# Performance work log

Measured on AMD Instinct MI355X. Metric: run time of the kernel, lower is better.

Reference implementation:

```python
import jax, jax.numpy as jnp
import numpy as np

# ---- static config (mirrors torch __init__ kwargs) ----
DIM, DEPTH, HEADS, DHEAD, MLP = 1024, 5, 8, 128, 2048
INNER = HEADS * DHEAD
RADIUS, K, SS, TKS, TS = 0.7, 16, 8, 3, 2
B, T, N = 2, 8, 2048
M = N // SS
JN = 17
EPS = 1e-5


def _ln(x, s, b):
    m = x.mean(-1, keepdims=True)
    v = ((x - m) ** 2).mean(-1, keepdims=True)
    return (x - m) * jax.lax.rsqrt(v + EPS) * s + b


def _fps(xyz, m):
    # farthest point sampling, pointnet2 semantics (first pick = index 0)
    # xyz: [BF, n, 3] -> [BF, m] int32
    BF, n, _ = xyz.shape
    d0 = jnp.full((BF, n), 1e10, xyz.dtype)
    i0 = jnp.zeros((BF,), jnp.int32)

    def body(carry, _):
        dist, last = carry
        p = jnp.take_along_axis(xyz, jnp.broadcast_to(last[:, None, None], (BF, 1, 3)), 1)
        dist = jnp.minimum(dist, jnp.sum((xyz - p) ** 2, -1))
        nxt = jnp.argmax(dist, -1).astype(jnp.int32)
        return (dist, nxt), nxt

    _, rest = jax.lax.scan(body, (d0, i0), None, length=m - 1)
    return jnp.concatenate([i0[None], rest], 0).T  # [BF, m]


def _forward(radar, conv_d_w, conv_f_w, pos_w, pos_b, joint_template, joint_pos,
             ln1_s, ln1_b, qkv_w, out_w, out_b, ln2_s, ln2_b,
             ff_w1, ff_b1, ff_w2, ff_b2,
             red_ln_s, red_ln_b, red_w1, red_b1, red_w2, red_b2,
             head_ln_s, head_ln_b, head_w1, head_b1, head_w2, head_b2):
    Bv = radar.shape[0]
    xyz, fea = radar[..., :3], radar[..., 3:]
    # ---- P4DConv tube embedding ----
    # temporal replicate padding [1, 0]
    xyz_p = jnp.concatenate([xyz[:, :1], xyz], 1)   # [B,T+1,N,3]
    fea_p = jnp.concatenate([fea[:, :1], fea], 1)
    centers = np.arange(1, (T + 1) - 1, TS)          # anchor frame indices (static)
    Tq = len(centers)
    offs = np.array([-1, 0, 1])                      # temporal kernel offsets (tks=3)
    cxyz = xyz_p[:, centers].reshape(Bv * Tq, N, 3)
    aidx = _fps(cxyz, M)                             # [B*Tq, M]
    anchors = jnp.take_along_axis(
        cxyz, jnp.broadcast_to(aidx[..., None], (Bv * Tq, M, 3)), 1
    ).reshape(Bv, Tq, M, 3)
    nx = jnp.stack([xyz_p[:, centers + o] for o in offs], 2)  # [B,Tq,3,N,3]
    nf = jnp.stack([fea_p[:, centers + o] for o in offs], 2)  # [B,Tq,3,N,3]
    # ball query: first-K indices with d2 < r^2 (in point order), padded with the
    # first hit; 0 if no hit -- matches pointnet2 CUDA semantics
    sg = jax.lax.stop_gradient
    d2 = jnp.sum((sg(anchors)[:, :, None, :, None, :] - sg(nx)[:, :, :, None, :, :]) ** 2, -1)
    cand = jnp.where(d2 < RADIUS ** 2, jnp.arange(N, dtype=jnp.int32), N)
    cand = jnp.sort(cand, -1)[..., :K]               # [B,Tq,3,M,K]
    first = cand[..., :1]
    idx = jnp.where(cand < N, cand, first)
    idx = jnp.where(first < N, idx, 0)
    BF = Bv * Tq * 3
    idxf = jnp.broadcast_to(idx.reshape(BF, M * K, 1), (BF, M * K, 3))
    gx = jnp.take_along_axis(nx.reshape(BF, N, 3), idxf, 1).reshape(Bv, Tq, 3, M, K, 3)
    gf = jnp.take_along_axis(nf.reshape(BF, N, 3), idxf, 1).reshape(Bv, Tq, 3, M, K, 3)
    disp = gx - anchors[:, :, None, :, None, :]
    tdisp = jnp.broadcast_to(
        jnp.asarray(offs, jnp.float32)[None, None, :, None, None, None],
        disp.shape[:-1] + (1,))
    # conv_d(displacement) + conv_f(features): fused single 1x1 conv (no bias)
    w = jnp.concatenate([conv_d_w, conv_f_w], 1)     # [DIM, 7]
    feat = jnp.einsum('btomkc,dc->btomkd', jnp.concatenate([disp, tdisp, gf], -1), w)
    feat = feat.max(4).max(2)                        # spatial max, temporal max -> [B,Tq,M,DIM]
    # ---- P4Transformer forward ----
    tt = jnp.broadcast_to(jnp.arange(1, Tq + 1, dtype=jnp.float32)[None, :, None, None],
                          (Bv, Tq, M, 1))
    xyzts = jnp.concatenate([anchors, tt], -1).reshape(Bv, Tq * M, 4)
    features = feat.reshape(Bv, Tq * M, DIM)
    emb = xyzts @ pos_w.T + pos_b + features         # pos_embedding is a 1x1 Conv1d
    joints = jnp.broadcast_to(joint_template[None] + joint_pos, (Bv, JN, DIM))
    x = jnp.concatenate([joints, emb], 1)            # [B, 17 + Tq*M, DIM]
    S = x.shape[1]
    scale = DHEAD ** -0.5
    for l in range(DEPTH):
        h = _ln(x, ln1_s[l], ln1_b[l])
        q, k, v = jnp.split(h @ qkv_w[l], 3, -1)
        q = q.reshape(Bv, S, HEADS, DHEAD).transpose(0, 2, 1, 3)
        k = k.reshape(Bv, S, HEADS, DHEAD).transpose(0, 2, 1, 3)
        v = v.reshape(Bv, S, HEADS, DHEAD).transpose(0, 2, 1, 3)
        att = jax.nn.softmax(jnp.einsum('bhid,bhjd->bhij', q, k) * scale, -1)
        o = jnp.einsum('bhij,bhjd->bhid', att, v).transpose(0, 2, 1, 3).reshape(Bv, S, INNER)
        x = x + o @ out_w[l] + out_b[l]
        h = _ln(x, ln2_s[l], ln2_b[l])
        x = x + jax.nn.gelu(h @ ff_w1[l] + ff_b1[l], approximate=False) @ ff_w2[l] + ff_b2[l]
    j = x[:, :JN]
    j64 = jax.nn.relu(_ln(j, red_ln_s, red_ln_b) @ red_w1 + red_b1) @ red_w2 + red_b2
    out = jax.nn.relu(_ln(j64, head_ln_s, head_ln_b) @ head_w1 + head_b1) @ head_w2 + head_b2
    # torch returns (output, None, joint_embed_out, radar_feature, radar_position);
    # None is dropped here
    return out, j64, features, xyzts


def setup_inputs():
    key = jax.random.key(0)
    ks = iter(jax.random.split(key, 40))

    def nrm(shape, fan_in):
        return jax.random.normal(next(ks), shape, jnp.float32) / float(np.sqrt(fan_in))

    inp = {}
    inp['radar'] = jax.random.normal(next(ks), (B, T, N, 6), jnp.float32)
    inp['conv_d_w'] = nrm((DIM, 4), 4)
    inp['conv_f_w'] = nrm((DIM, 3), 3)
    inp['pos_w'] = nrm((DIM, 4), 4)
    inp['pos_b'] = jnp.zeros((DIM,), jnp.float32)
    inp['joint_template'] = jax.random.uniform(next(ks), (JN, DIM), jnp.float32)
    i = np.arange(JN)[:, None]
    j = np.arange(DIM)[None, :]
    ang = i / 10000.0 ** ((j - (j % 2)) / DIM)
    inp['joint_pos'] = jnp.asarray(np.where(j % 2 == 0, np.sin(ang), np.cos(ang))[None],
                                   jnp.float32)
    inp['ln1_s'] = jnp.ones((DEPTH, DIM), jnp.float32)
    inp['ln1_b'] = jnp.zeros((DEPTH, DIM), jnp.float32)
    inp['qkv_w'] = nrm((DEPTH, DIM, 3 * INNER), DIM)
    inp['out_w'] = nrm((DEPTH, INNER, DIM), INNER)
    inp['out_b'] = jnp.zeros((DEPTH, DIM), jnp.float32)
    inp['ln2_s'] = jnp.ones((DEPTH, DIM), jnp.float32)
    inp['ln2_b'] = jnp.zeros((DEPTH, DIM), jnp.float32)
    inp['ff_w1'] = nrm((DEPTH, DIM, MLP), DIM)
    inp['ff_b1'] = jnp.zeros((DEPTH, MLP), jnp.float32)
    inp['ff_w2'] = nrm((DEPTH, MLP, DIM), MLP)
    inp['ff_b2'] = jnp.zeros((DEPTH, DIM), jnp.float32)
    inp['red_ln_s'] = jnp.ones((DIM,), jnp.float32)
    inp['red_ln_b'] = jnp.zeros((DIM,), jnp.float32)
    inp['red_w1'] = nrm((DIM, 512), DIM)
    inp['red_b1'] = jnp.zeros((512,), jnp.float32)
    inp['red_w2'] = nrm((512, 64), 512)
    inp['red_b2'] = jnp.zeros((64,), jnp.float32)
    inp['head_ln_s'] = jnp.ones((64,), jnp.float32)
    inp['head_ln_b'] = jnp.zeros((64,), jnp.float32)
    inp['head_w1'] = nrm((64, 32), 64)
    inp['head_b1'] = jnp.zeros((32,), jnp.float32)
    inp['head_w2'] = nrm((32, 3), 32)
    inp['head_b2'] = jnp.zeros((3,), jnp.float32)
    return inp


def reference(radar, conv_d_w, conv_f_w, pos_w, pos_b, joint_template, joint_pos,
              ln1_s, ln1_b, qkv_w, out_w, out_b, ln2_s, ln2_b,
              ff_w1, ff_b1, ff_w2, ff_b2,
              red_ln_s, red_ln_b, red_w1, red_b1, red_w2, red_b2,
              head_ln_s, head_ln_b, head_w1, head_b1, head_w2, head_b2):
    return _forward(radar, conv_d_w, conv_f_w, pos_w, pos_b, joint_template, joint_pos,
                    ln1_s, ln1_b, qkv_w, out_w, out_b, ln2_s, ln2_b,
                    ff_w1, ff_b1, ff_w2, ff_b2,
                    red_ln_s, red_ln_b, red_w1, red_b1, red_w2, red_b2,
                    head_ln_s, head_ln_b, head_w1, head_b1, head_w2, head_b2)
```

## Files before the change

kernel.cpp:

```cpp
#include <hip/hip_runtime.h>
#include <hip/hip_bf16.h>

#define S_LEN 1041
#define ROWS  2082

__device__ __forceinline__ float d2chain(float dx, float dy, float dz) {
  float t = dx * dx;
  t = fmaf(dy, dy, t);
  t = fmaf(dz, dz, t);
  return t;
}

__device__ __forceinline__ float gelu_exact(float v) {
  return 0.5f * v * (1.0f + erff(v * 0.70710678118654752f));
}

__global__ __launch_bounds__(256) void fps_kernel(const float* __restrict__ radar,
                                                  float* __restrict__ anchors,
                                                  float* __restrict__ xyzts) {
  __shared__ float xs[2048], ys[2048], zs[2048];
  __shared__ int warr[256];
  __shared__ float rv[4];
  __shared__ int ri[4];
  int bf = blockIdx.x;
  int b = bf >> 2, tq = bf & 3;
  int f = 2 * tq;
  const float* base = radar + (size_t)(b * 8 + f) * 2048 * 6;
  int tid = threadIdx.x;
#pragma unroll
  for (int r = 0; r < 8; ++r) {
    int n = tid + r * 256;
    const float* p = base + (size_t)n * 6;
    xs[n] = p[0]; ys[n] = p[1]; zs[n] = p[2];
  }
  float dist[8];
#pragma unroll
  for (int r = 0; r < 8; ++r) dist[r] = 1e10f;
  if (tid == 0) warr[0] = 0;
  __syncthreads();
  int last = 0;
  for (int it = 1; it < 256; ++it) {
    float px = xs[last], py = ys[last], pz = zs[last];
    float bv = -1.0f; int bi = 0x7fffffff;
#pragma unroll
    for (int r = 0; r < 8; ++r) {
      int n = tid + r * 256;
      float d = fminf(dist[r], d2chain(xs[n] - px, ys[n] - py, zs[n] - pz));
      dist[r] = d;
      if (d > bv || (d == bv && n < bi)) { bv = d; bi = n; }
    }
#pragma unroll
    for (int o = 1; o < 64; o <<= 1) {
      float ov = __shfl_xor(bv, o);
      int   oi = __shfl_xor(bi, o);
      if (ov > bv || (ov == bv && oi < bi)) { bv = ov; bi = oi; }
    }
    if ((tid & 63) == 0) { rv[tid >> 6] = bv; ri[tid >> 6] = bi; }
    __syncthreads();
    if (tid == 0) {
      float fv = rv[0]; int fi = ri[0];
      for (int w = 1; w < 4; ++w)
        if (rv[w] > fv || (rv[w] == fv && ri[w] < fi)) { fv = rv[w]; fi = ri[w]; }
      warr[it] = fi;
    }
    __syncthreads();
    last = warr[it];
  }
  int m = tid;
  int a = warr[m];
  float ax = xs[a], ay = ys[a], az = zs[a];
  float* ap = anchors + (size_t)(bf * 256 + m) * 3;
  ap[0] = ax; ap[1] = ay; ap[2] = az;
  float* xp = xyzts + (size_t)(b * 1024 + tq * 256 + m) * 4;
  xp[0] = ax; xp[1] = ay; xp[2] = az; xp[3] = (float)(tq + 1);
}

__global__ __launch_bounds__(256) void radius_kernel(const float* __restrict__ radar,
                                                     const float* __restrict__ anchors,
                                                     int* __restrict__ nidx) {
  int r = blockIdx.x * 256 + threadIdx.x;
  int m = r & 255;
  int g = r >> 8;
  int o = g % 3;
  int bt = g / 3;
  int tq = bt & 3, b = bt >> 2;
  const float* ap = anchors + (size_t)(bt * 256 + m) * 3;
  float ax = ap[0], ay = ap[1], az = ap[2];
  int u = 2 * tq + o;
  int f = (u == 0) ? 0 : (u - 1);
  const float* base = radar + (size_t)(b * 8 + f) * 2048 * 6;
  size_t ob = (size_t)r * 16;
  int cnt = 0, first = 0;
  for (int n = 0; n < 2048; ++n) {
    const float* p = base + (size_t)n * 6;
    float t = d2chain(ax - p[0], ay - p[1], az - p[2]);
    if (t < 0.49f) {
      if (cnt == 0) first = n;
      nidx[ob + cnt] = n;
      if (++cnt == 16) break;
    }
  }
  for (int k = cnt; k < 16; ++k) nidx[ob + k] = first;
}

__global__ __launch_bounds__(256) void group_kernel(const float* __restrict__ radar,
                                                    const float* __restrict__ anchors,
                                                    const int* __restrict__ nidx,
                                                    const float* __restrict__ cdw,
                                                    const float* __restrict__ cfw,
                                                    const float* __restrict__ posw,
                                                    const float* __restrict__ posb,
                                                    float* __restrict__ feat,
                                                    float* __restrict__ x) {
  __shared__ float in7[48][8];
  int blk = blockIdx.x;
  int m = blk & 255, bt = blk >> 8;
  int tq = bt & 3, b = bt >> 2;
  int tid = threadIdx.x;
  float a0 = anchors[(size_t)blk * 3 + 0];
  float a1 = anchors[(size_t)blk * 3 + 1];
  float a2 = anchors[(size_t)blk * 3 + 2];
  if (tid < 48) {
    int o = tid >> 4;
    int k = tid & 15;
    int gi = nidx[((size_t)(bt * 3 + o) * 256 + m) * 16 + k];
    int u = 2 * tq + o;
    int f = (u == 0) ? 0 : (u - 1);
    const float* p = radar + ((size_t)(b * 8 + f) * 2048 + gi) * 6;
    in7[tid][0] = p[0] - a0;
    in7[tid][1] = p[1] - a1;
    in7[tid][2] = p[2] - a2;
    in7[tid][3] = (float)(o - 1);
    in7[tid][4] = p[3];
    in7[tid][5] = p[4];
    in7[tid][6] = p[5];
  }
  __syncthreads();
  float tt = (float)(tq + 1);
#pragma unroll
  for (int j = 0; j < 4; ++j) {
    int d = j * 256 + tid;
    float4 wd = *(const float4*)(cdw + (size_t)d * 4);
    float w4 = cfw[(size_t)d * 3 + 0];
    float w5 = cfw[(size_t)d * 3 + 1];
    float w6 = cfw[(size_t)d * 3 + 2];
    float best = -INFINITY;
    for (int c = 0; c < 48; ++c) {
      const float* e = in7[c];
      float t = e[0] * wd.x;
      t = fmaf(e[1], wd.y, t);
      t = fmaf(e[2], wd.z, t);
      t = fmaf(e[3], wd.w, t);
      t = fmaf(e[4], w4, t);
      t = fmaf(e[5], w5, t);
      t = fmaf(e[6], w6, t);
      best = fmaxf(best, t);
    }
    feat[(size_t)blk * 1024 + d] = best;
    float4 pw = *(const float4*)(posw + (size_t)d * 4);
    float e = fmaf(a0, pw.x, fmaf(a1, pw.y, fmaf(a2, pw.z, fmaf(tt, pw.w, posb[d]))));
    x[((size_t)(b * 1041 + 17) + tq * 256 + m) * 1024 + d] = e + best;
  }
}

__global__ __launch_bounds__(256) void joints_kernel(const float* __restrict__ jt,
                                                     const float* __restrict__ jp,
                                                     float* __restrict__ x) {
  int blk = blockIdx.x;
  int b = blk / 17, jj = blk % 17;
  int d = threadIdx.x * 4;
  float4 t = *(const float4*)(jt + (size_t)jj * 1024 + d);
  float4 p = *(const float4*)(jp + (size_t)jj * 1024 + d);
  float4 r;
  r.x = t.x + p.x; r.y = t.y + p.y; r.z = t.z + p.z; r.w = t.w + p.w;
  *(float4*)(x + ((size_t)(b * 1041 + jj)) * 1024 + d) = r;
}

__global__ __launch_bounds__(256) void ln_kernel(const float* __restrict__ x,
                                                 const float* __restrict__ s,
                                                 const float* __restrict__ b,
                                                 float* __restrict__ h) {
  __shared__ float red[8];
  int row = blockIdx.x;
  int tid = threadIdx.x;
  float4 v = *(const float4*)(x + (size_t)row * 1024 + tid * 4);
  float sum = (v.x + v.y) + (v.z + v.w);
#pragma unroll
  for (int o = 32; o > 0; o >>= 1) sum += __shfl_xor(sum, o);
  if ((tid & 63) == 0) red[tid >> 6] = sum;
  __syncthreads();
  float mean = (red[0] + red[1] + red[2] + red[3]) * (1.0f / 1024.0f);
  float dx = v.x - mean, dy = v.y - mean, dz = v.z - mean, dw = v.w - mean;
  float sq = (dx * dx + dy * dy) + (dz * dz + dw * dw);
#pragma unroll
  for (int o = 32; o > 0; o >>= 1) sq += __shfl_xor(sq, o);
  if ((tid & 63) == 0) red[4 + (tid >> 6)] = sq;
  __syncthreads();
  float var = (red[4] + red[5] + red[6] + red[7]) * (1.0f / 1024.0f);
  float rs = rsqrtf(var + 1e-5f);
  float4 sv = *(const float4*)(s + tid * 4);
  float4 bv = *(const float4*)(b + tid * 4);
  float4 out;
  out.x = dx * rs * sv.x + bv.x;
  out.y = dy * rs * sv.y + bv.y;
  out.z = dz * rs * sv.z + bv.z;
  out.w = dw * rs * sv.w + bv.w;
  *(float4*)(h + (size_t)row * 1024 + tid * 4) = out;
}

template <bool BIAS, bool RES, bool GACT>
__global__ __launch_bounds__(256) void gemm64(const float* __restrict__ A,
                                              const float* __restrict__ Bw,
                                              const float* __restrict__ bias,
                                              float* __restrict__ C,
                                              int M, int N, int K) {
  __shared__ float As[16][68];
  __shared__ float Bs[16][132];
  int tid = threadIdx.x;
  int tx = tid & 15, ty = tid >> 4;
  int m0 = blockIdx.y * 64, n0 = blockIdx.x * 128;
  float acc[4][8] = {};
  int arow = tid >> 2, ak = (tid & 3) * 4;
  int brow = tid >> 4, bcol = (tid & 15) * 8;
  bool aok = (m0 + arow) < M;
  const float* aptr = A + (size_t)(m0 + arow) * K + ak;
  const float* bptr = Bw + (size_t)brow * N + n0 + bcol;
  for (int k0 = 0; k0 < K; k0 += 16) {
    float4 av = aok ? *(const float4*)(aptr + k0) : make_float4(0.f, 0.f, 0.f, 0.f);
    float4 b0 = *(const float4*)(bptr + (size_t)k0 * N);
    float4 b1 = *(const float4*)(bptr + (size_t)k0 * N + 4);
    __syncthreads();
    As[ak + 0][arow] = av.x;
    As[ak + 1][arow] = av.y;
    As[ak + 2][arow] = av.z;
    As[ak + 3][arow] = av.w;
    *(float4*)&Bs[brow][bcol] = b0;
    *(float4*)&Bs[brow][bcol + 4] = b1;
    __syncthreads();
#pragma unroll
    for (int kk = 0; kk < 16; ++kk) {
      float4 a4 = *(const float4*)&As[kk][ty * 4];
      float4 x0 = *(const float4*)&Bs[kk][tx * 8];
      float4 x1 = *(const float4*)&Bs[kk][tx * 8 + 4];
      float am[4] = {a4.x, a4.y, a4.z, a4.w};
      float bn[8] = {x0.x, x0.y, x0.z, x0.w, x1.x, x1.y, x1.z, x1.w};
#pragma unroll
      for (int i = 0; i < 4; ++i)
#pragma unroll
        for (int j = 0; j < 8; ++j) acc[i][j] = fmaf(am[i], bn[j], acc[i][j]);
    }
  }
#pragma unroll
  for (int i = 0; i < 4; ++i) {
    int row = m0 + ty * 4 + i;
    if (row < M) {
      float* cp = C + (size_t)row * N + n0 + tx * 8;
#pragma unroll
      for (int j = 0; j < 8; ++j) {
        float v = acc[i][j];
        if (BIAS) v += bias[n0 + tx * 8 + j];
        if (GACT) v = gelu_exact(v);
        if (RES) v += cp[j];
        cp[j] = v;
      }
    }
  }
}

__global__ __launch_bounds__(256) void attn_kernel(const float* __restrict__ qkv,
                                                   float* __restrict__ o) {
  __shared__ float Ks[32][128];
  __shared__ float Vs[32][128];
  __shared__ float Sl[32][33];
  int bh = blockIdx.y;
  int b = bh >> 3, hh = bh & 7;
  int tid = threadIdx.x;
  int g = tid >> 3, l8 = tid & 7;
  int qi = blockIdx.x * 32 + g;
  bool qok = qi < S_LEN;
  const float* base = qkv + (size_t)b * S_LEN * 3072;
  float qv[16];
  if (qok) {
    const float4* qp = (const float4*)(base + (size_t)qi * 3072 + hh * 128 + l8 * 16);
    float4 q0 = qp[0], q1 = qp[1], q2 = qp[2], q3 = qp[3];
    qv[0] = q0.x; qv[1] = q0.y; qv[2] = q0.z; qv[3] = q0.w;
    qv[4] = q1.x; qv[5] = q1.y; qv[6] = q1.z; qv[7] = q1.w;
    qv[8] = q2.x; qv[9] = q2.y; qv[10] = q2.z; qv[11] = q2.w;
    qv[12] = q3.x; qv[13] = q3.y; qv[14] = q3.z; qv[15] = q3.w;
  } else {
#pragma unroll
    for (int j = 0; j < 16; ++j) qv[j] = 0.f;
  }
  float ov[16];
#pragma unroll
  for (int j = 0; j < 16; ++j) ov[j] = 0.f;
  float mrun = -INFINITY, lrun = 0.f;
  const float scale = 0.08838834764831845f;
  for (int j0 = 0; j0 < S_LEN; j0 += 32) {
    __syncthreads();
#pragma unroll
    for (int r = 0; r < 4; ++r) {
      int f4 = r * 256 + tid;
      int key = f4 >> 5;
      int c4 = (f4 & 31) * 4;
      int jj = j0 + key;
      float4 kv, vv;
      if (jj < S_LEN) {
        kv = *(const float4*)(base + (size_t)jj * 3072 + 1024 + hh * 128 + c4);
        vv = *(const float4*)(base + (size_t)jj * 3072 + 2048 + hh * 128 + c4);
      } else {
        kv = make_float4(0.f, 0.f, 0.f, 0.f);
        vv = make_float4(0.f, 0.f, 0.f, 0.f);
      }
      *(float4*)&Ks[key][c4] = kv;
      *(float4*)&Vs[key][c4] = vv;
    }
    __syncthreads();
    float tmax = -INFINITY;
    for (int jj = 0; jj < 32; ++jj) {
      const float* kr = &Ks[jj][l8 * 16];
      float4 k0 = *(const float4*)(kr);
      float4 k1 = *(const float4*)(kr + 4);
      float4 k2 = *(const float4*)(kr + 8);
      float4 k3 = *(const float4*)(kr + 12);
      float s0 = qv[0] * k0.x; s0 = fmaf(qv[1], k0.y, s0); s0 = fmaf(qv[2], k0.z, s0); s0 = fmaf(qv[3], k0.w, s0);
      float s1 = qv[4] * k1.x; s1 = fmaf(qv[5], k1.y, s1); s1 = fmaf(qv[6], k1.z, s1); s1 = fmaf(qv[7], k1.w, s1);
      float s2 = qv[8] * k2.x; s2 = fmaf(qv[9], k2.y, s2); s2 = fmaf(qv[10], k2.z, s2); s2 = fmaf(qv[11], k2.w, s2);
      float s3 = qv[12] * k3.x; s3 = fmaf(qv[13], k3.y, s3); s3 = fmaf(qv[14], k3.z, s3); s3 = fmaf(qv[15], k3.w, s3);
      float s = (s0 + s1) + (s2 + s3);
      s += __shfl_xor(s, 1);
      s += __shfl_xor(s, 2);
      s += __shfl_xor(s, 4);
      s *= scale;
      if (j0 + jj >= S_LEN) s = -INFINITY;
      if (l8 == (jj & 7)) Sl[g][jj] = s;
      tmax = fmaxf(tmax, s);
    }
    __syncthreads();
    float mnew = fmaxf(mrun, tmax);
    float corr = expf(mrun - mnew);
    lrun *= corr;
#pragma unroll
    for (int j = 0; j < 16; ++j) ov[j] *= corr;
    for (int jj = 0; jj < 32; ++jj) {
      float p = expf(Sl[g][jj] - mnew);
      lrun += p;
      const float* vr = &Vs[jj][l8 * 16];
      float4 v0 = *(const float4*)(vr);
      float4 v1 = *(const float4*)(vr + 4);
      float4 v2 = *(const float4*)(vr + 8);
      float4 v3 = *(const float4*)(vr + 12);
      ov[0] = fmaf(p, v0.x, ov[0]);  ov[1] = fmaf(p, v0.y, ov[1]);
      ov[2] = fmaf(p, v0.z, ov[2]);  ov[3] = fmaf(p, v0.w, ov[3]);
      ov[4] = fmaf(p, v1.x, ov[4]);  ov[5] = fmaf(p, v1.y, ov[5]);
      ov[6] = fmaf(p, v1.z, ov[6]);  ov[7] = fmaf(p, v1.w, ov[7]);
      ov[8] = fmaf(p, v2.x, ov[8]);  ov[9] = fmaf(p, v2.y, ov[9]);
      ov[10] = fmaf(p, v2.z, ov[10]); ov[11] = fmaf(p, v2.w, ov[11]);
      ov[12] = fmaf(p, v3.x, ov[12]); ov[13] = fmaf(p, v3.y, ov[13]);
      ov[14] = fmaf(p, v3.z, ov[14]); ov[15] = fmaf(p, v3.w, ov[15]);
    }
    mrun = mnew;
  }
  if (qok) {
    float inv = 1.0f / lrun;
    float* op = o + ((size_t)(b * S_LEN + qi)) * 1024 + hh * 128 + l8 * 16;
#pragma unroll
    for (int j = 0; j < 16; ++j) op[j] = ov[j] * inv;
  }
}

__global__ __launch_bounds__(256) void red_kernel(const float* __restrict__ x,
                                                  const float* __restrict__ lns,
                                                  const float* __restrict__ lnb,
                                                  const float* __restrict__ w1,
                                                  const float* __restrict__ b1,
                                                  const float* __restrict__ w2,
                                                  const float* __restrict__ b2,
                                                  float* __restrict__ j64) {
  __shared__ float row[1024];
  __shared__ float hid[512];
  __shared__ float red[8];
  int blk = blockIdx.x;
  int b = blk / 17, jj = blk % 17;
  int tid = threadIdx.x;
  float4 v = *(const float4*)(x + ((size_t)(b * 1041 + jj)) * 1024 + tid * 4);
  float sum = (v.x + v.y) + (v.z + v.w);
#pragma unroll
  for (int o = 32; o > 0; o >>= 1) sum += __shfl_xor(sum, o);
  if ((tid & 63) == 0) red[tid >> 6] = sum;
  __syncthreads();
  float mean = (red[0] + red[1] + red[2] + red[3]) * (1.0f / 1024.0f);
  float dx = v.x - mean, dy = v.y - mean, dz = v.z - mean, dw = v.w - mean;
  float sq = (dx * dx + dy * dy) + (dz * dz + dw * dw);
#pragma unroll
  for (int o = 32; o > 0; o >>= 1) sq += __shfl_xor(sq, o);
  if ((tid & 63) == 0) red[4 + (tid >> 6)] = sq;
  __syncthreads();
  float var = (red[4] + red[5] + red[6] + red[7]) * (1.0f / 1024.0f);
  float rs = rsqrtf(var + 1e-5f);
  float4 sv = *(const float4*)(lns + tid * 4);
  float4 bv = *(const float4*)(lnb + tid * 4);
  row[tid * 4 + 0] = dx * rs * sv.x + bv.x;
  row[tid * 4 + 1] = dy * rs * sv.y + bv.y;
  row[tid * 4 + 2] = dz * rs * sv.z + bv.z;
  row[tid * 4 + 3] = dw * rs * sv.w + bv.w;
  __syncthreads();
  for (int u = tid; u < 512; u += 256) {
    float acc = 0.f;
    for (int c = 0; c < 1024; ++c) acc = fmaf(row[c], w1[(size_t)c * 512 + u], acc);
    hid[u] = fmaxf(acc + b1[u], 0.f);
  }
  __syncthreads();
  if (tid < 64) {
    float acc = 0.f;
    for (int c = 0; c < 512; ++c) acc = fmaf(hid[c], w2[(size_t)c * 64 + tid], acc);
    j64[(size_t)blk * 64 + tid] = acc + b2[tid];
  }
}

__global__ __launch_bounds__(64) void head_kernel(const float* __restrict__ j64,
                                                  const float* __restrict__ lns,
                                                  const float* __restrict__ lnb,
                                                  const float* __restrict__ w1,
                                                  const float* __restrict__ b1,
                                                  const float* __restrict__ w2,
                                                  const float* __restrict__ b2,
                                                  float* __restrict__ outp) {
  __shared__ float nb[64];
  __shared__ float hid[32];
  int blk = blockIdx.x;
  int tid = threadIdx.x;
  float v = j64[(size_t)blk * 64 + tid];
  float sum = v;
#pragma unroll
  for (int o = 32; o > 0; o >>= 1) sum += __shfl_xor(sum, o);
  float mean = sum * (1.0f / 64.0f);
  float d = v - mean;
  float sq = d * d;
#pragma unroll
  for (int o = 32; o > 0; o >>= 1) sq += __shfl_xor(sq, o);
  float var = sq * (1.0f / 64.0f);
  float rs = rsqrtf(var + 1e-5f);
  nb[tid] = d * rs * lns[tid] + lnb[tid];
  __syncthreads();
  if (tid < 32) {
    float acc = 0.f;
    for (int c = 0; c < 64; ++c) acc = fmaf(nb[c], w1[c * 32 + tid], acc);
    hid[tid] = fmaxf(acc + b1[tid], 0.f);
  }
  __syncthreads();
  if (tid < 3) {
    float acc = 0.f;
    for (int c = 0; c < 32; ++c) acc = fmaf(hid[c], w2[c * 3 + tid], acc);
    outp[(size_t)blk * 3 + tid] = acc + b2[tid];
  }
}

extern "C" void kernel_launch(void* const* d_in, const int* in_sizes, int n_in,
                              void* d_out, int out_size, void* d_ws, size_t ws_size,
                              hipStream_t stream) {
  const float* radar = (const float*)d_in[0];
  const float* cdw   = (const float*)d_in[1];
  const float* cfw   = (const float*)d_in[2];
  const float* posw  = (const float*)d_in[3];
  const float* posb  = (const float*)d_in[4];
  const float* jt    = (const float*)d_in[5];
  const float* jp    = (const float*)d_in[6];
  const float* ln1s  = (const float*)d_in[7];
  const float* ln1b  = (const float*)d_in[8];
  const float* qkvw  = (const float*)d_in[9];
  const float* outw  = (const float*)d_in[10];
  const float* outb  = (const float*)d_in[11];
  const float* ln2s  = (const float*)d_in[12];
  const float* ln2b  = (const float*)d_in[13];
  const float* ffw1  = (const float*)d_in[14];
  const float* ffb1  = (const float*)d_in[15];
  const float* ffw2  = (const float*)d_in[16];
  const float* ffb2  = (const float*)d_in[17];
  const float* rlns  = (const float*)d_in[18];
  const float* rlnb  = (const float*)d_in[19];
  const float* rw1   = (const float*)d_in[20];
  const float* rb1   = (const float*)d_in[21];
  const float* rw2   = (const float*)d_in[22];
  const float* rb2   = (const float*)d_in[23];
  const float* hlns  = (const float*)d_in[24];
  const float* hlnb  = (const float*)d_in[25];
  const float* hw1   = (const float*)d_in[26];
  const float* hb1   = (const float*)d_in[27];
  const float* hw2   = (const float*)d_in[28];
  const float* hb2   = (const float*)d_in[29];

  float* out0      = (float*)d_out;
  float* out_j64   = out0 + 102;
  float* out_feat  = out_j64 + 2176;
  float* out_xyzts = out_feat + 2097152;

  float* anchors = (float*)d_ws;
  int*   nidx    = (int*)((char*)d_ws + 6144 * 4);
  float* xbuf    = (float*)((char*)d_ws + (6144 + 98304) * 4);
  float* hbuf    = xbuf + (size_t)ROWS * 1024;
  float* big     = hbuf + (size_t)ROWS * 1024;
  if (ws_size < 43057152u) return;

  fps_kernel<<<8, 256, 0, stream>>>(radar, anchors, out_xyzts);
  radius_kernel<<<24, 256, 0, stream>>>(radar, anchors, nidx);
  group_kernel<<<2048, 256, 0, stream>>>(radar, anchors, nidx, cdw, cfw, posw, posb,
                                         out_feat, xbuf);
  joints_kernel<<<34, 256, 0, stream>>>(jt, jp, xbuf);

  for (int l = 0; l < 5; ++l) {
    ln_kernel<<<ROWS, 256, 0, stream>>>(xbuf, ln1s + l * 1024, ln1b + l * 1024, hbuf);
    gemm64<false, false, false><<<dim3(24, 33), 256, 0, stream>>>(
        hbuf, qkvw + (size_t)l * 1024 * 3072, nullptr, big, ROWS, 3072, 1024);
    attn_kernel<<<dim3(33, 16), 256, 0, stream>>>(big, hbuf);
    gemm64<true, true, false><<<dim3(8, 33), 256, 0, stream>>>(
        hbuf, outw + (size_t)l * 1024 * 1024, outb + l * 1024, xbuf, ROWS, 1024, 1024);
    ln_kernel<<<ROWS, 256, 0, stream>>>(xbuf, ln2s + l * 1024, ln2b + l * 1024, hbuf);
    gemm64<true, false, true><<<dim3(16, 33), 256, 0, stream>>>(
        hbuf, ffw1 + (size_t)l * 1024 * 2048, ffb1 + l * 2048, big, ROWS, 2048, 1024);
    gemm64<true, true, false><<<dim3(8, 33), 256, 0, stream>>>(
        big, ffw2 + (size_t)l * 2048 * 1024, ffb2 + l * 1024, xbuf, ROWS, 1024, 2048);
  }

  red_kernel<<<34, 256, 0, stream>>>(xbuf, rlns, rlnb, rw1, rb1, rw2, rb2, out_j64);
  head_kernel<<<34, 64, 0, stream>>>(out_j64, hlns, hlnb, hw1, hb1, hw2, hb2, out0);
}
```

Measured before the change: 7.591 ms.

## Use split-bf16 MFMA GEMMs and narrow attention query groups

Replaces the FP32 SIMT GEMM with a 128x128-tile MFMA GEMM. It emulates FP32 precision by splitting A and W into bf16 high and low parts and issuing three MFMAs per tile. Each weight matrix is converted per layer into an MFMA-fragment layout by a new wconv kernel, adding a conversion pass and extra workspace. The attention kernel now uses 16 lanes per query and 16 queries per block, which doubles the grid, and it drops one barrier. The aim is to move the dominant GEMM cost onto matrix cores and raise attention occupancy, at the cost of conversion overhead and some precision risk.

```diff
diff --git a/kernel.cpp b/kernel.cpp
--- a/kernel.cpp
+++ b/kernel.cpp
@@ -3,6 +3,23 @@
 
 #define S_LEN 1041
 #define ROWS  2082
+
+typedef __attribute__((ext_vector_type(8))) short bs8;
+typedef __attribute__((ext_vector_type(4))) float f32x4;
+
+union U8 { bs8 v; unsigned short u[8]; uint4 q; };
+
+__device__ __forceinline__ unsigned short f2bf(float x) {
+  unsigned int u = __float_as_uint(x);
+  return (unsigned short)((u + 0x7FFFu + ((u >> 16) & 1u)) >> 16);
+}
+__device__ __forceinline__ float bf2f(unsigned short h) {
+  return __uint_as_float(((unsigned int)h) << 16);
+}
+
+__device__ __forceinline__ f32x4 mfma16(bs8 a, bs8 b, f32x4 c) {
+  return __builtin_amdgcn_mfma_f32_16x16x32_bf16(a, b, c, 0, 0, 0);
+}
 
 __device__ __forceinline__ float d2chain(float dx, float dy, float dz) {
   float t = dx * dx;
@@ -208,60 +225,119 @@
   *(float4*)(h + (size_t)row * 1024 + tid * 4) = out;
 }
 
+__global__ __launch_bounds__(256) void wconv(const float* __restrict__ W,
+                                             unsigned short* __restrict__ out,
+                                             int K, int N) {
+  int tid = threadIdx.x;
+  int l = tid & 63, w = tid >> 6;
+  int kb = blockIdx.y;
+  int K32 = K >> 5;
+  size_t plane = (size_t)K * N;
+#pragma unroll
+  for (int t = 0; t < 2; ++t) {
+    int nt = blockIdx.x * 8 + w * 2 + t;
+    int col = nt * 16 + (l & 15);
+    int krow = kb * 32 + ((l >> 4) << 3);
+    U8 h, lo;
+#pragma unroll
+    for (int j = 0; j < 8; ++j) {
+      float xv = W[(size_t)(krow + j) * N + col];
+      unsigned short hb = f2bf(xv);
+      h.u[j] = hb;
+      lo.u[j] = f2bf(xv - bf2f(hb));
+    }
+    size_t idx = (((size_t)nt * K32 + kb) * 64 + l) * 8;
+    *(uint4*)(out + idx) = h.q;
+    *(uint4*)(out + plane + idx) = lo.q;
+  }
+}
+
 template <bool BIAS, bool RES, bool GACT>
-__global__ __launch_bounds__(256) void gemm64(const float* __restrict__ A,
-                                              const float* __restrict__ Bw,
-                                              const float* __restrict__ bias,
-                                              float* __restrict__ C,
-                                              int M, int N, int K) {
-  __shared__ float As[16][68];
-  __shared__ float Bs[16][132];
-  int tid = threadIdx.x;
-  int tx = tid & 15, ty = tid >> 4;
-  int m0 = blockIdx.y * 64, n0 = blockIdx.x * 128;
-  float acc[4][8] = {};
-  int arow = tid >> 2, ak = (tid & 3) * 4;
-  int brow = tid >> 4, bcol = (tid & 15) * 8;
-  bool aok = (m0 + arow) < M;
-  const float* aptr = A + (size_t)(m0 + arow) * K + ak;
-  const float* bptr = Bw + (size_t)brow * N + n0 + bcol;
-  for (int k0 = 0; k0 < K; k0 += 16) {
-    float4 av = aok ? *(const float4*)(aptr + k0) : make_float4(0.f, 0.f, 0.f, 0.f);
-    float4 b0 = *(const float4*)(bptr + (size_t)k0 * N);
-    float4 b1 = *(const float4*)(bptr + (size_t)k0 * N + 4);
+__global__ __launch_bounds__(256) void mgemm(const float* __restrict__ A,
+                                             const unsigned short* __restrict__ Wf,
+                                             const float* __restrict__ bias,
+                                             float* __restrict__ C,
+                                             int M, int N, int K) {
+  __shared__ uint4 sA[2][8][64];
+  __shared__ uint4 sB[2][8][64];
+  int tid = threadIdx.x;
+  int l = tid & 63, w = tid >> 6;
+  int wm = w >> 1, wn = w & 1;
+  int m0 = blockIdx.y * 128, n0 = blockIdx.x * 128;
+  int K32 = K >> 5;
+  size_t plane = (size_t)K * N;
+  f32x4 acc[4][4] = {};
+  for (int k0 = 0; k0 < K32; ++k0) {
+#pragma unroll
+    for (int s = 0; s < 2; ++s) {
+      int mt = w + s * 4;
+      int row = m0 + mt * 16 + (l & 15);
+      int kb = (k0 << 5) + ((l >> 4) << 3);
+      float v[8];
+      if (row < M) {
+        float4 p0 = *(const float4*)(A + (size_t)row * K + kb);
+        float4 p1 = *(const float4*)(A + (size_t)row * K + kb + 4);
+        v[0] = p0.x; v[1] = p0.y; v[2] = p0.z; v[3] = p0.w;
+        v[4] = p1.x; v[5] = p1.y; v[6] = p1.z; v[7] = p1.w;
+      } else {
+#pragma unroll
+        for (int j = 0; j < 8; ++j) v[j] = 0.f;
+      }
+      U8 h, lo;
+#pragma unroll
+      for (int j = 0; j < 8; ++j) {
+        unsigned short hb = f2bf(v[j]);
+        h.u[j] = hb;
+        lo.u[j] = f2bf(v[j] - bf2f(hb));
+      }
+      sA[0][mt][l] = h.q;
+      sA[1][mt][l] = lo.q;
+    }
+#pragma unroll
+    for (int s2 = 0; s2 < 4; ++s2) {
+      int seg = w * 4 + s2;
+      int ntl = seg >> 1, ver = seg & 1;
+      int ntg = (n0 >> 4) + ntl;
+      size_t gidx = (((size_t)ntg * K32 + k0) * 64 + l) * 8 + (ver ? plane : 0);
+      sB[ver][ntl][l] = *(const uint4*)(Wf + gidx);
+    }
     __syncthreads();
-    As[ak + 0][arow] = av.x;
-    As[ak + 1][arow] = av.y;
-    As[ak + 2][arow] = av.z;
-    As[ak + 3][arow] = av.w;
-    *(float4*)&Bs[brow][bcol] = b0;
-    *(float4*)&Bs[brow][bcol + 4] = b1;
+    U8 ah[4], al[4], bh[4], bl[4];
+#pragma unroll
+    for (int i = 0; i < 4; ++i) {
+      ah[i].q = sA[0][wm * 4 + i][l];
+      al[i].q = sA[1][wm * 4 + i][l];
+      bh[i].q = sB[0][wn * 4 + i][l];
+      bl[i].q = sB[1][wn * 4 + i][l];
+    }
+#pragma unroll
+    for (int i = 0; i < 4; ++i)
+#pragma unroll
+      for (int j = 0; j < 4; ++j) {
+        acc[i][j] = mfma16(ah[i].v, bh[j].v, acc[i][j]);
+        acc[i][j] = mfma16(al[i].v, bh[j].v, acc[i][j]);
+        acc[i][j] = mfma16(ah[i].v, bl[j].v, acc[i][j]);
+      }
     __syncthreads();
-#pragma unroll
-    for (int kk = 0; kk < 16; ++kk) {
-      float4 a4 = *(const float4*)&As[kk][ty * 4];
-      float4 x0 = *(const float4*)&Bs[kk][tx * 8];
-      float4 x1 = *(const float4*)&Bs[kk][tx * 8 + 4];
-      float am[4] = {a4.x, a4.y, a4.z, a4.w};
-      float bn[8] = {x0.x, x0.y, x0.z, x0.w, x1.x, x1.y, x1.z, x1.w};
-#pragma unroll
-      for (int i = 0; i < 4; ++i)
-#pragma unroll
-        for (int j = 0; j < 8; ++j) acc[i][j] = fmaf(am[i], bn[j], acc[i][j]);
-    }
   }
 #pragma unroll
   for (int i = 0; i < 4; ++i) {
-    int row = m0 + ty * 4 + i;
-    if (row < M) {
-      float* cp = C + (size_t)row * N + n0 + tx * 8;
-#pragma unroll
-      for (int j = 0; j < 8; ++j) {
-        float v = acc[i][j];
-        if (BIAS) v += bias[n0 + tx * 8 + j];
-        if (GACT) v = gelu_exact(v);
-        if (RES) v += cp[j];
-        cp[j] = v;
+    int rbase = m0 + wm * 64 + i * 16 + ((l >> 4) << 2);
+#pragma unroll
+    for (int j = 0; j < 4; ++j) {
+      int col = n0 + wn * 64 + j * 16 + (l & 15);
+      f32x4 c = acc[i][j];
+#pragma unroll
+      for (int reg = 0; reg < 4; ++reg) {
+        int row = rbase + reg;
+        if (row < M) {
+          float v = c[reg];
+          if (BIAS) v += bias[col];
+          if (GACT) v = gelu_exact(v);
+          float* cp = C + (size_t)row * N + col;
+          if (RES) v += *cp;
+          *cp = v;
+        }
       }
     }
   }
@@ -271,29 +347,27 @@
                                                    float* __restrict__ o) {
   __shared__ float Ks[32][128];
   __shared__ float Vs[32][128];
-  __shared__ float Sl[32][33];
+  __shared__ float Sl[16][33];
   int bh = blockIdx.y;
   int b = bh >> 3, hh = bh & 7;
   int tid = threadIdx.x;
-  int g = tid >> 3, l8 = tid & 7;
-  int qi = blockIdx.x * 32 + g;
+  int g = tid >> 4, l16 = tid & 15;
+  int qi = blockIdx.x * 16 + g;
   bool qok = qi < S_LEN;
   const float* base = qkv + (size_t)b * S_LEN * 3072;
-  float qv[16];
+  float qv[8];
   if (qok) {
-    const float4* qp = (const float4*)(base + (size_t)qi * 3072 + hh * 128 + l8 * 16);
-    float4 q0 = qp[0], q1 = qp[1], q2 = qp[2], q3 = qp[3];
+    float4 q0 = *(const float4*)(base + (size_t)qi * 3072 + hh * 128 + l16 * 4);
+    float4 q1 = *(const float4*)(base + (size_t)qi * 3072 + hh * 128 + 64 + l16 * 4);
     qv[0] = q0.x; qv[1] = q0.y; qv[2] = q0.z; qv[3] = q0.w;
     qv[4] = q1.x; qv[5] = q1.y; qv[6] = q1.z; qv[7] = q1.w;
-    qv[8] = q2.x; qv[9] = q2.y; qv[10] = q2.z; qv[11] = q2.w;
-    qv[12] = q3.x; qv[13] = q3.y; qv[14] = q3.z; qv[15] = q3.w;
   } else {
 #pragma unroll
-    for (int j = 0; j < 16; ++j) qv[j] = 0.f;
-  }
-  float ov[16];
-#pragma unroll
-  for (int j = 0; j < 16; ++j) ov[j] = 0.f;
+    for (int j = 0; j < 8; ++j) qv[j] = 0.f;
+  }
+  float ov[8];
+#pragma unroll
+  for (int j = 0; j < 8; ++j) ov[j] = 0.f;
   float mrun = -INFINITY, lrun = 0.f;
   const float scale = 0.08838834764831845f;
   for (int j0 = 0; j0 < S_LEN; j0 += 32) {
@@ -318,54 +392,47 @@
     __syncthreads();
     float tmax = -INFINITY;
     for (int jj = 0; jj < 32; ++jj) {
-      const float* kr = &Ks[jj][l8 * 16];
-      float4 k0 = *(const float4*)(kr);
-      float4 k1 = *(const float4*)(kr + 4);
-      float4 k2 = *(const float4*)(kr + 8);
-      float4 k3 = *(const float4*)(kr + 12);
-      float s0 = qv[0] * k0.x; s0 = fmaf(qv[1], k0.y, s0); s0 = fmaf(qv[2], k0.z, s0); s0 = fmaf(qv[3], k0.w, s0);
-      float s1 = qv[4] * k1.x; s1 = fmaf(qv[5], k1.y, s1); s1 = fmaf(qv[6], k1.z, s1); s1 = fmaf(qv[7], k1.w, s1);
-      float s2 = qv[8] * k2.x; s2 = fmaf(qv[9], k2.y, s2); s2 = fmaf(qv[10], k2.z, s2); s2 = fmaf(qv[11], k2.w, s2);
-      float s3 = qv[12] * k3.x; s3 = fmaf(qv[13], k3.y, s3); s3 = fmaf(qv[14], k3.z, s3); s3 = fmaf(qv[15], k3.w, s3);
-      float s = (s0 + s1) + (s2 + s3);
+      float4 k0 = *(const float4*)&Ks[jj][l16 * 4];
+      float4 k1 = *(const float4*)&Ks[jj][64 + l16 * 4];
+      float s0 = qv[0] * k0.x; s0 = fmaf(qv[1], k0.y, s0);
+      s0 = fmaf(qv[2], k0.z, s0); s0 = fmaf(qv[3], k0.w, s0);
+      float s1 = qv[4] * k1.x; s1 = fmaf(qv[5], k1.y, s1);
+      s1 = fmaf(qv[6], k1.z, s1); s1 = fmaf(qv[7], k1.w, s1);
+      float s = s0 + s1;
       s += __shfl_xor(s, 1);
       s += __shfl_xor(s, 2);
       s += __shfl_xor(s, 4);
+      s += __shfl_xor(s, 8);
       s *= scale;
       if (j0 + jj >= S_LEN) s = -INFINITY;
-      if (l8 == (jj & 7)) Sl[g][jj] = s;
+      if (l16 == (jj & 15)) Sl[g][jj] = s;
       tmax = fmaxf(tmax, s);
     }
-    __syncthreads();
     float mnew = fmaxf(mrun, tmax);
     float corr = expf(mrun - mnew);
     lrun *= corr;
 #pragma unroll
-    for (int j = 0; j < 16; ++j) ov[j] *= corr;
+    for (int j = 0; j < 8; ++j) ov[j] *= corr;
     for (int jj = 0; jj < 32; ++jj) {
       float p = expf(Sl[g][jj] - mnew);
       lrun += p;
-      const float* vr = &Vs[jj][l8 * 16];
-      float4 v0 = *(const float4*)(vr);
-      float4 v1 = *(const float4*)(vr + 4);
-      float4 v2 = *(const float4*)(vr + 8);
-      float4 v3 = *(const float4*)(vr + 12);
-      ov[0] = fmaf(p, v0.x, ov[0]);  ov[1] = fmaf(p, v0.y, ov[1]);
-      ov[2] = fmaf(p, v0.z, ov[2]);  ov[3] = fmaf(p, v0.w, ov[3]);
-      ov[4] = fmaf(p, v1.x, ov[4]);  ov[5] = fmaf(p, v1.y, ov[5]);
-      ov[6] = fmaf(p, v1.z, ov[6]);  ov[7] = fmaf(p, v1.w, ov[7]);
-      ov[8] = fmaf(p, v2.x, ov[8]);  ov[9] = fmaf(p, v2.y, ov[9]);
-      ov[10] = fmaf(p, v2.z, ov[10]); ov[11] = fmaf(p, v2.w, ov[11]);
-      ov[12] = fmaf(p, v3.x, ov[12]); ov[13] = fmaf(p, v3.y, ov[13]);
-      ov[14] = fmaf(p, v3.z, ov[14]); ov[15] = fmaf(p, v3.w, ov[15]);
+      float4 v0 = *(const float4*)&Vs[jj][l16 * 4];
+      float4 v1 = *(const float4*)&Vs[jj][64 + l16 * 4];
+      ov[0] = fmaf(p, v0.x, ov[0]); ov[1] = fmaf(p, v0.y, ov[1]);
+      ov[2] = fmaf(p, v0.z, ov[2]); ov[3] = fmaf(p, v0.w, ov[3]);
+      ov[4] = fmaf(p, v1.x, ov[4]); ov[5] = fmaf(p, v1.y, ov[5]);
+      ov[6] = fmaf(p, v1.z, ov[6]); ov[7] = fmaf(p, v1.w, ov[7]);
     }
     mrun = mnew;
   }
   if (qok) {
     float inv = 1.0f / lrun;
-    float* op = o + ((size_t)(b * S_LEN + qi)) * 1024 + hh * 128 + l8 * 16;
-#pragma unroll
-    for (int j = 0; j < 16; ++j) op[j] = ov[j] * inv;
+    float* op = o + ((size_t)(b * S_LEN + qi)) * 1024 + hh * 128;
+    float4 o0, o1;
+    o0.x = ov[0] * inv; o0.y = ov[1] * inv; o0.z = ov[2] * inv; o0.w = ov[3] * inv;
+    o1.x = ov[4] * inv; o1.y = ov[5] * inv; o1.z = ov[6] * inv; o1.w = ov[7] * inv;
+    *(float4*)(op + l16 * 4) = o0;
+    *(float4*)(op + 64 + l16 * 4) = o1;
   }
 }
 
@@ -500,7 +567,8 @@
   float* xbuf    = (float*)((char*)d_ws + (6144 + 98304) * 4);
   float* hbuf    = xbuf + (size_t)ROWS * 1024;
   float* big     = hbuf + (size_t)ROWS * 1024;
-  if (ws_size < 43057152u) return;
+  unsigned short* wbuf = (unsigned short*)(big + (size_t)ROWS * 3072);
+  if (ws_size < 55640064u) return;
 
   fps_kernel<<<8, 256, 0, stream>>>(radar, anchors, out_xyzts);
   radius_kernel<<<24, 256, 0, stream>>>(radar, anchors, nidx);
@@ -510,16 +578,20 @@
 
   for (int l = 0; l < 5; ++l) {
     ln_kernel<<<ROWS, 256, 0, stream>>>(xbuf, ln1s + l * 1024, ln1b + l * 1024, hbuf);
-    gemm64<false, false, false><<<dim3(24, 33), 256, 0, stream>>>(
-        hbuf, qkvw + (size_t)l * 1024 * 3072, nullptr, big, ROWS, 3072, 1024);
-    attn_kernel<<<dim3(33, 16), 256, 0, stream>>>(big, hbuf);
-    gemm64<true, true, false><<<dim3(8, 33), 256, 0, stream>>>(
-        hbuf, outw + (size_t)l * 1024 * 1024, outb + l * 1024, xbuf, ROWS, 1024, 1024);
+    wconv<<<dim3(24, 32), 256, 0, stream>>>(qkvw + (size_t)l * 1024 * 3072, wbuf, 1024, 3072);
+    mgemm<false, false, false><<<dim3(24, 17), 256, 0, stream>>>(
+        hbuf, wbuf, nullptr, big, ROWS, 3072, 1024);
+    attn_kernel<<<dim3(66, 16), 256, 0, stream>>>(big, hbuf);
+    wconv<<<dim3(8, 32), 256, 0, stream>>>(outw + (size_t)l * 1024 * 1024, wbuf, 1024, 1024);
+    mgemm<true, true, false><<<dim3(8, 17), 256, 0, stream>>>(
+        hbuf, wbuf, outb + l * 1024, xbuf, ROWS, 1024, 1024);
     ln_kernel<<<ROWS, 256, 0, stream>>>(xbuf, ln2s + l * 1024, ln2b + l * 1024, hbuf);
-    gemm64<true, false, true><<<dim3(16, 33), 256, 0, stream>>>(
-        hbuf, ffw1 + (size_t)l * 1024 * 2048, ffb1 + l * 2048, big, ROWS, 2048, 1024);
-    gemm64<true, true, false><<<dim3(8, 33), 256, 0, stream>>>(
-        big, ffw2 + (size_t)l * 2048 * 1024, ffb2 + l * 1024, xbuf, ROWS, 1024, 2048);
+    wconv<<<dim3(16, 32), 256, 0, stream>>>(ffw1 + (size_t)l * 1024 * 2048, wbuf, 1024, 2048);
+    mgemm<true, false, true><<<dim3(16, 17), 256, 0, stream>>>(
+        hbuf, wbuf, ffb1 + l * 2048, big, ROWS, 2048, 1024);
+    wconv<<<dim3(8, 64), 256, 0, stream>>>(ffw2 + (size_t)l * 2048 * 1024, wbuf, 2048, 1024);
+    mgemm<true, true, false><<<dim3(8, 17), 256, 0, stream>>>(
+        big, wbuf, ffb2 + l * 1024, xbuf, ROWS, 1024, 2048);
   }
 
   red_kernel<<<34, 256, 0, stream>>>(xbuf, rlns, rlnb, rw1, rb1, rw2, rb2, out_j64);
```

Measured after the change: 6.733 ms. 1.13x faster.
